# Kernel optimization log

Measured on AMD Instinct MI355X. Metric: run time of the kernel, lower is better.

## Reference

```python
import jax, jax.numpy as jnp
import numpy as np

B, P, S, D, H, DFF, VOC = 16, 10, 128, 512, 8, 2048, 32000
SIGMA = 0.05
LN_EPS = 1e-6


def _ln(x, g, b):
    mu = jnp.mean(x, axis=-1, keepdims=True)
    var = jnp.var(x, axis=-1, keepdims=True)
    return g * (x - mu) / jnp.sqrt(var + LN_EPS) + b


def setup_inputs() -> dict:
    key = jax.random.key(0)
    ks = jax.random.split(key, 16)
    def wmat(k, shp):
        return (jax.random.normal(k, shp) * 0.02).astype(jnp.float32)
    return {
        "r": jax.random.normal(ks[0], (B, P, D), jnp.float32),
        "x": jax.random.randint(ks[1], (B,), 0, VOC),
        "K": jax.random.normal(ks[2], (B, P, S, D), jnp.float32),
        "V": jax.random.normal(ks[3], (B, P, S, D), jnp.float32),
        "w_state": jax.random.uniform(ks[4], (B, P, 1), jnp.float32),
        "I": jax.random.randint(ks[5], (B, P, S), 0, P),
        "t": 64,
        "Wq": wmat(ks[6], (D, D)), "bq": jnp.zeros((D,), jnp.float32),
        "Wk": wmat(ks[7], (D, D)), "bk": jnp.zeros((D,), jnp.float32),
        "Wv": wmat(ks[8], (D, D)), "bv": jnp.zeros((D,), jnp.float32),
        "Wo": wmat(ks[9], (D, D)), "bo": jnp.zeros((D,), jnp.float32),
        "W1": wmat(ks[10], (D, DFF)), "b1": jnp.zeros((DFF,), jnp.float32),
        "W2": wmat(ks[11], (DFF, D)), "b2": jnp.zeros((D,), jnp.float32),
        "g1": jnp.ones((D,), jnp.float32), "be1": jnp.zeros((D,), jnp.float32),
        "g3": jnp.ones((D,), jnp.float32), "be3": jnp.zeros((D,), jnp.float32),
        "Wout": wmat(ks[12], (D, VOC)), "bout": jnp.zeros((VOC,), jnp.float32),
    }


def reference(r, x, K, V, w_state, I, t, Wq, bq, Wk, bk, Wv, bv, Wo, bo,
              W1, b1, W2, b2, g1, be1, g3, be3, Wout, bout):
    k1, k2, k3, k4, k5 = jax.random.split(jax.random.key(42), 5)
    I = I.astype(jnp.int32)
    # particle resampling of attention state: gather along particle dim per timestep
    K = jnp.take_along_axis(K, I[..., None], axis=1)  # (B,P,S,D)
    V = jnp.take_along_axis(V, I[..., None], axis=1)
    rin = r[:, :, None, :]                            # (B,P,1,D)
    q = rin @ Wq + bq
    k = rin @ Wk + bk
    v = rin @ Wv + bv
    # SMC reparameterization noise on the projections
    q = q + SIGMA * jax.random.normal(k1, q.shape, q.dtype)
    k = k + SIGMA * jax.random.normal(k2, k.shape, k.dtype)
    v = v + SIGMA * jax.random.normal(k3, v.shape, v.dtype)
    # write current k, v into the attention state at position t
    K = jax.lax.dynamic_update_slice_in_dim(K, k, t, axis=2)
    V = jax.lax.dynamic_update_slice_in_dim(V, v, t, axis=2)
    dh = D // H
    qh = q.reshape(B, P, 1, H, dh).transpose(0, 1, 3, 2, 4)  # (B,P,H,1,dh)
    Kh = K.reshape(B, P, S, H, dh).transpose(0, 1, 3, 2, 4)  # (B,P,H,S,dh)
    Vh = V.reshape(B, P, S, H, dh).transpose(0, 1, 3, 2, 4)
    scores = jnp.einsum('bphqd,bphsd->bphqs', qh, Kh) / jnp.sqrt(jnp.asarray(dh, q.dtype))
    attn = jax.nn.softmax(scores, axis=-1)                   # (B,P,H,1,S)
    ctx = jnp.einsum('bphqs,bphsd->bphqd', attn, Vh)
    ctx = ctx.transpose(0, 1, 3, 2, 4).reshape(B, P, 1, D)
    z = ctx @ Wo + bo
    epsilon = SIGMA * jax.random.normal(k4, z.shape, z.dtype)  # stored stddev
    z = z + epsilon
    attn_weights = jnp.mean(attn, axis=2)                    # (B,P,1,S)
    out1 = _ln(z + rin, g1, be1)
    ffn = jax.nn.relu(out1 @ W1 + b1) @ W2 + b2
    out3 = _ln(ffn + out1, g3, be3)                          # (B,P,1,D)
    predictions = out3 @ Wout + bout                         # (B,P,1,VOC)
    # classification weight computation: softmax + gather at label x
    probs = jax.nn.softmax(predictions, axis=-1)
    w = jnp.take_along_axis(probs, x[:, None, None, None].astype(jnp.int32), axis=-1)[..., 0, 0]  # (B,P)
    w = jax.lax.stop_gradient(w)
    pred_sq = predictions[:, :, 0, :]                        # (B,P,VOC)
    average_prediction = jnp.sum(pred_sq * w[:, :, None], axis=1)[:, None, :]  # (B,1,VOC)
    argmax_w = jnp.argmax(w, axis=1)
    max_prediction = jnp.take_along_axis(pred_sq, argmax_w[:, None, None], axis=1)[:, 0, :]  # (B,VOC)
    # sample-and-keep-indices: categorical draw of P particle ancestors per batch
    i_t = jax.random.categorical(k5, w[:, None, :], axis=-1, shape=(B, P)).astype(jnp.int32)
    I_new = jax.lax.dynamic_update_slice_in_dim(I, i_t[:, :, None], t, axis=2)
    I_new = jax.lax.stop_gradient(I_new)
    # resample z with the freshly-sampled indices (I_new[:,:,t] == i_t)
    z = jnp.take_along_axis(z, i_t[:, :, None, None], axis=1)
    return out3, z, average_prediction, max_prediction, epsilon, attn_weights, K, V, w, I_new
```

## Files before the change

kernel.cpp:

```cpp
#include <hip/hip_runtime.h>
#include <cstdint>
#include <cstddef>

#define B_    16
#define P_    10
#define S_    128
#define D_    512
#define H_    8
#define DH_   64
#define DFF_  2048
#define VOC_  32000
#define NROW  160
#define SIGMA 0.05f
#define LN_EPS 1e-6f

struct U2 { uint32_t x, y; };

__host__ __device__ __forceinline__ U2 tf2x32(uint32_t k0, uint32_t k1,
                                              uint32_t x0, uint32_t x1) {
  uint32_t ks[3] = {k0, k1, k0 ^ k1 ^ 0x1BD11BDAu};
  x0 += ks[0]; x1 += ks[1];
  const int R0[4] = {13, 15, 26, 6};
  const int R1[4] = {17, 29, 16, 24};
#pragma unroll
  for (int i = 0; i < 5; ++i) {
    const int* r = (i & 1) ? R1 : R0;
#pragma unroll
    for (int j = 0; j < 4; ++j) {
      x0 += x1;
      x1 = (x1 << r[j]) | (x1 >> (32 - r[j]));
      x1 ^= x0;
    }
    x0 += ks[(i + 1) % 3];
    x1 += ks[(i + 2) % 3] + (uint32_t)(i + 1);
  }
  return {x0, x1};
}

__device__ __forceinline__ uint32_t jax_bits32(uint32_t k0, uint32_t k1, uint32_t j) {
  U2 o = tf2x32(k0, k1, 0u, j);
  return o.x ^ o.y;
}

__device__ __forceinline__ float erfinv32(float x) {
  float w = -log1pf(-x * x);
  float p;
  if (w < 5.0f) {
    w = w - 2.5f;
    p = 2.81022636e-08f;
    p = fmaf(p, w, 3.43273939e-07f);
    p = fmaf(p, w, -3.5233877e-06f);
    p = fmaf(p, w, -4.39150654e-06f);
    p = fmaf(p, w, 0.00021858087f);
    p = fmaf(p, w, -0.00125372503f);
    p = fmaf(p, w, -0.00417768164f);
    p = fmaf(p, w, 0.246640727f);
    p = fmaf(p, w, 1.50140941f);
  } else {
    w = sqrtf(w) - 3.0f;
    p = -0.000200214257f;
    p = fmaf(p, w, 0.000100950558f);
    p = fmaf(p, w, 0.00134934322f);
    p = fmaf(p, w, -0.00367342844f);
    p = fmaf(p, w, 0.00573950773f);
    p = fmaf(p, w, -0.0076224613f);
    p = fmaf(p, w, 0.00943887047f);
    p = fmaf(p, w, 1.00167406f);
    p = fmaf(p, w, 2.83297682f);
  }
  return p * x;
}

__device__ __forceinline__ float jax_normal(uint32_t k0, uint32_t k1, uint32_t j) {
  uint32_t b = jax_bits32(k0, k1, j);
  float u01 = __uint_as_float((b >> 9) | 0x3F800000u) - 1.0f;
  const float lo = -0.99999994f;
  float u = fmaxf(lo, fmaf(u01, 2.0f, lo));
  return 1.41421356f * erfinv32(u);
}

__device__ __forceinline__ float jax_gumbel(uint32_t k0, uint32_t k1, uint32_t j) {
  uint32_t b = jax_bits32(k0, k1, j);
  float u01 = __uint_as_float((b >> 9) | 0x3F800000u) - 1.0f;
  const float tiny = 1.17549435e-38f;
  float u = fmaxf(tiny, u01 + tiny);
  return -logf(-logf(u));
}


__global__ __launch_bounds__(256) void k_gather(const float* __restrict__ K,
                                                const float* __restrict__ V,
                                                const int* __restrict__ I,
                                                float* __restrict__ oK,
                                                float* __restrict__ oV) {
  size_t idx = (size_t)blockIdx.x * 256 + threadIdx.x;
  const size_t total = (size_t)NROW * S_ * (D_ / 4);
  if (idx >= total) return;
  int d4 = (int)(idx % (D_ / 4));
  size_t row = idx / (D_ / 4);
  int s = (int)(row % S_);
  int bp = (int)(row / S_);
  int b = bp / P_;
  int iv = I[row];
  size_t src = ((size_t)(b * P_ + iv) * S_ + s) * (D_ / 4) + d4;
  ((float4*)oK)[idx] = ((const float4*)K)[src];
  ((float4*)oV)[idx] = ((const float4*)V)[src];
}

__global__ __launch_bounds__(128) void k_qkvp(const float* __restrict__ r,
    const float* __restrict__ Wq, const float* __restrict__ bq,
    const float* __restrict__ Wk, const float* __restrict__ bk,
    const float* __restrict__ Wv, const float* __restrict__ bv,
    float* __restrict__ pq, float* __restrict__ pk, float* __restrict__ pv) {
  int c = blockIdx.x * 128 + threadIdx.x;
  int r0 = blockIdx.y * 4;
  int kc = blockIdx.z;
  int d0 = kc * 64;
  float aq[4], ak[4], av[4];
  float bbq = (kc == 0) ? bq[c] : 0.f;
  float bbk = (kc == 0) ? bk[c] : 0.f;
  float bbv = (kc == 0) ? bv[c] : 0.f;
#pragma unroll
  for (int rr = 0; rr < 4; ++rr) { aq[rr] = bbq; ak[rr] = bbk; av[rr] = bbv; }
  for (int d = d0; d < d0 + 64; d += 4) {
    float wq0 = Wq[(size_t)d * D_ + c],      wq1 = Wq[(size_t)(d+1) * D_ + c];
    float wq2 = Wq[(size_t)(d+2) * D_ + c],  wq3 = Wq[(size_t)(d+3) * D_ + c];
    float wk0 = Wk[(size_t)d * D_ + c],      wk1 = Wk[(size_t)(d+1) * D_ + c];
    float wk2 = Wk[(size_t)(d+2) * D_ + c],  wk3 = Wk[(size_t)(d+3) * D_ + c];
    float wv0 = Wv[(size_t)d * D_ + c],      wv1 = Wv[(size_t)(d+1) * D_ + c];
    float wv2 = Wv[(size_t)(d+2) * D_ + c],  wv3 = Wv[(size_t)(d+3) * D_ + c];
#pragma unroll
    for (int rr = 0; rr < 4; ++rr) {
      float4 a = *(const float4*)&r[(size_t)(r0 + rr) * D_ + d];
      aq[rr] = fmaf(a.w, wq3, fmaf(a.z, wq2, fmaf(a.y, wq1, fmaf(a.x, wq0, aq[rr]))));
      ak[rr] = fmaf(a.w, wk3, fmaf(a.z, wk2, fmaf(a.y, wk1, fmaf(a.x, wk0, ak[rr]))));
      av[rr] = fmaf(a.w, wv3, fmaf(a.z, wv2, fmaf(a.y, wv1, fmaf(a.x, wv0, av[rr]))));
    }
  }
#pragma unroll
  for (int rr = 0; rr < 4; ++rr) {
    size_t o = ((size_t)kc * NROW + r0 + rr) * D_ + c;
    pq[o] = aq[rr]; pk[o] = ak[rr]; pv[o] = av[rr];
  }
}

__global__ __launch_bounds__(256) void k_qkvr(const float* __restrict__ pq,
    const float* __restrict__ pk, const float* __restrict__ pv,
    const int* __restrict__ tptr, float* __restrict__ wsq,
    float* __restrict__ oK, float* __restrict__ oV,
    uint32_t k1a, uint32_t k1b, uint32_t k2a, uint32_t k2b,
    uint32_t k3a, uint32_t k3b) {
  int idx = blockIdx.x * 256 + threadIdx.x;
  if (idx >= NROW * D_) return;
  float q = pq[idx], k = pk[idx], v = pv[idx];
#pragma unroll
  for (int kc = 1; kc < 8; ++kc) {
    size_t o = (size_t)kc * (NROW * D_) + idx;
    q += pq[o]; k += pk[o]; v += pv[o];
  }
  int bp = idx / D_, c = idx % D_;
  int ts = min(max(*tptr, 0), S_ - 1);
  uint32_t j = (uint32_t)idx;
  wsq[idx] = q + SIGMA * jax_normal(k1a, k1b, j);
  oK[((size_t)bp * S_ + ts) * D_ + c] = k + SIGMA * jax_normal(k2a, k2b, j);
  oV[((size_t)bp * S_ + ts) * D_ + c] = v + SIGMA * jax_normal(k3a, k3b, j);
}

__global__ __launch_bounds__(128) void k_attn(const float* __restrict__ wsq,
    const float* __restrict__ oK, const float* __restrict__ oV,
    float* __restrict__ wsctx, float* __restrict__ wsattn) {
  __shared__ float s_q[DH_];
  __shared__ float s_attn[S_];
  __shared__ float red[S_];
  int bp = blockIdx.x >> 3, h = blockIdx.x & 7, tid = threadIdx.x;
  if (tid < DH_) s_q[tid] = wsq[bp * D_ + h * DH_ + tid];
  __syncthreads();
  const float4* krow = (const float4*)(oK + ((size_t)bp * S_ + tid) * D_ + h * DH_);
  const float4* q4 = (const float4*)s_q;
  float sc = 0.f;
#pragma unroll
  for (int d = 0; d < DH_ / 4; ++d) {
    float4 kv = krow[d], qv = q4[d];
    sc += qv.x * kv.x + qv.y * kv.y + qv.z * kv.z + qv.w * kv.w;
  }
  sc *= 0.125f;
  red[tid] = sc; __syncthreads();
  for (int s = 64; s > 0; s >>= 1) {
    if (tid < s) red[tid] = fmaxf(red[tid], red[tid + s]);
    __syncthreads();
  }
  float m = red[0]; __syncthreads();
  float e = expf(sc - m);
  red[tid] = e; __syncthreads();
  for (int s = 64; s > 0; s >>= 1) {
    if (tid < s) red[tid] += red[tid + s];
    __syncthreads();
  }
  float a = e / red[0];
  s_attn[tid] = a;
  wsattn[(size_t)blockIdx.x * S_ + tid] = a;
  __syncthreads();
  {
    int dd = tid & 63, sh = tid >> 6;
    const float* vb = oV + ((size_t)bp * S_ + sh * 64) * D_ + h * DH_ + dd;
    float acc = 0.f;
#pragma unroll 4
    for (int s = 0; s < 64; ++s) acc = fmaf(s_attn[sh * 64 + s], vb[(size_t)s * D_], acc);
    red[tid] = acc; __syncthreads();
    if (tid < DH_) wsctx[bp * D_ + h * DH_ + tid] = red[tid] + red[tid + 64];
  }
}

__global__ __launch_bounds__(256) void k_aw(const float* __restrict__ wsattn,
                                            float* __restrict__ oaw) {
  int idx = blockIdx.x * 256 + threadIdx.x;
  if (idx >= NROW * S_) return;
  int bp = idx / S_, s = idx % S_;
  float acc = 0.f;
#pragma unroll
  for (int h = 0; h < H_; ++h) acc += wsattn[(size_t)(bp * H_ + h) * S_ + s];
  oaw[idx] = acc * 0.125f;
}

__global__ __launch_bounds__(128) void k_zmatp(const float* __restrict__ wsctx,
    const float* __restrict__ Wo, const float* __restrict__ bo,
    float* __restrict__ pz) {
  int c = blockIdx.x * 128 + threadIdx.x;
  int r0 = blockIdx.y * 4;
  int kc = blockIdx.z;
  int d0 = kc * 64;
  float acc[4];
  float bb = (kc == 0) ? bo[c] : 0.f;
#pragma unroll
  for (int rr = 0; rr < 4; ++rr) acc[rr] = bb;
  for (int d = d0; d < d0 + 64; d += 4) {
    float w0 = Wo[(size_t)d * D_ + c],     w1 = Wo[(size_t)(d+1) * D_ + c];
    float w2 = Wo[(size_t)(d+2) * D_ + c], w3 = Wo[(size_t)(d+3) * D_ + c];
#pragma unroll
    for (int rr = 0; rr < 4; ++rr) {
      float4 a = *(const float4*)&wsctx[(size_t)(r0 + rr) * D_ + d];
      acc[rr] = fmaf(a.w, w3, fmaf(a.z, w2, fmaf(a.y, w1, fmaf(a.x, w0, acc[rr]))));
    }
  }
#pragma unroll
  for (int rr = 0; rr < 4; ++rr)
    pz[((size_t)kc * NROW + r0 + rr) * D_ + c] = acc[rr];
}

__global__ __launch_bounds__(256) void k_zmatr(const float* __restrict__ pz,
    const float* __restrict__ r, float* __restrict__ oeps,
    float* __restrict__ wsz, float* __restrict__ wsx,
    uint32_t k4a, uint32_t k4b) {
  int idx = blockIdx.x * 256 + threadIdx.x;
  if (idx >= NROW * D_) return;
  float s = pz[idx];
#pragma unroll
  for (int kc = 1; kc < 8; ++kc) s += pz[(size_t)kc * (NROW * D_) + idx];
  uint32_t j = (uint32_t)idx;
  float eps = SIGMA * jax_normal(k4a, k4b, j);
  oeps[idx] = eps;
  float z = s + eps;
  wsz[idx] = z;
  wsx[idx] = z + r[idx];
}

__global__ __launch_bounds__(256) void k_ln(const float* __restrict__ wsx,
    const float* __restrict__ g, const float* __restrict__ b,
    float* __restrict__ o) {
  __shared__ float red[256];
  int bp = blockIdx.x, tid = threadIdx.x;
  float x0 = wsx[bp * D_ + tid], x1 = wsx[bp * D_ + tid + 256];
  red[tid] = x0 + x1; __syncthreads();
  for (int s = 128; s > 0; s >>= 1) { if (tid < s) red[tid] += red[tid + s]; __syncthreads(); }
  float mu = red[0] / (float)D_; __syncthreads();
  float d0 = x0 - mu, d1 = x1 - mu;
  red[tid] = d0 * d0 + d1 * d1; __syncthreads();
  for (int s = 128; s > 0; s >>= 1) { if (tid < s) red[tid] += red[tid + s]; __syncthreads(); }
  float inv = 1.0f / sqrtf(red[0] / (float)D_ + LN_EPS);
  o[bp * D_ + tid] = g[tid] * d0 * inv + b[tid];
  o[bp * D_ + tid + 256] = g[tid + 256] * d1 * inv + b[tid + 256];
}

__global__ __launch_bounds__(128) void k_ffn1p(const float* __restrict__ wsout1,
    const float* __restrict__ W1, const float* __restrict__ b1,
    float* __restrict__ pf) {
  int c = blockIdx.x * 128 + threadIdx.x;
  int r0 = blockIdx.y * 8;
  int kc = blockIdx.z;
  int d0 = kc * 128;
  float acc[8];
  float bb = (kc == 0) ? b1[c] : 0.f;
#pragma unroll
  for (int rr = 0; rr < 8; ++rr) acc[rr] = bb;
  for (int d = d0; d < d0 + 128; d += 4) {
    float w0 = W1[(size_t)d * DFF_ + c],     w1 = W1[(size_t)(d+1) * DFF_ + c];
    float w2 = W1[(size_t)(d+2) * DFF_ + c], w3 = W1[(size_t)(d+3) * DFF_ + c];
#pragma unroll
    for (int rr = 0; rr < 8; ++rr) {
      float4 a = *(const float4*)&wsout1[(size_t)(r0 + rr) * D_ + d];
      acc[rr] = fmaf(a.w, w3, fmaf(a.z, w2, fmaf(a.y, w1, fmaf(a.x, w0, acc[rr]))));
    }
  }
#pragma unroll
  for (int rr = 0; rr < 8; ++rr)
    pf[((size_t)kc * NROW + r0 + rr) * DFF_ + c] = acc[rr];
}

__global__ __launch_bounds__(256) void k_ffn1r(const float* __restrict__ pf,
    float* __restrict__ wsffn) {
  int idx = blockIdx.x * 256 + threadIdx.x;
  if (idx >= NROW * DFF_) return;
  float s = pf[idx];
#pragma unroll
  for (int kc = 1; kc < 4; ++kc) s += pf[(size_t)kc * (NROW * DFF_) + idx];
  wsffn[idx] = fmaxf(s, 0.f);
}

__global__ __launch_bounds__(128) void k_ffn2p(const float* __restrict__ wsffn,
    const float* __restrict__ W2, float* __restrict__ p2) {
  int c = blockIdx.x * 128 + threadIdx.x;
  int r0 = blockIdx.y * 4;
  int kc = blockIdx.z;
  int d0 = kc * 128;
  float acc[4];
#pragma unroll
  for (int rr = 0; rr < 4; ++rr) acc[rr] = 0.f;
  for (int d = d0; d < d0 + 128; d += 4) {
    float w0 = W2[(size_t)d * D_ + c],     w1 = W2[(size_t)(d+1) * D_ + c];
    float w2 = W2[(size_t)(d+2) * D_ + c], w3 = W2[(size_t)(d+3) * D_ + c];
#pragma unroll
    for (int rr = 0; rr < 4; ++rr) {
      float4 a = *(const float4*)&wsffn[(size_t)(r0 + rr) * DFF_ + d];
      acc[rr] = fmaf(a.w, w3, fmaf(a.z, w2, fmaf(a.y, w1, fmaf(a.x, w0, acc[rr]))));
    }
  }
#pragma unroll
  for (int rr = 0; rr < 4; ++rr)
    p2[((size_t)kc * NROW + r0 + rr) * D_ + c] = acc[rr];
}

__global__ __launch_bounds__(256) void k_ffn2r(const float* __restrict__ p2,
    const float* __restrict__ b2, const float* __restrict__ wsout1,
    float* __restrict__ wsx) {
  int idx = blockIdx.x * 256 + threadIdx.x;
  if (idx >= NROW * D_) return;
  float s = p2[idx];
#pragma unroll
  for (int kc = 1; kc < 16; ++kc) s += p2[(size_t)kc * (NROW * D_) + idx];
  int c = idx % D_;
  wsx[idx] = s + b2[c] + wsout1[idx];
}

__global__ __launch_bounds__(256, 3) void k_preds(const float* __restrict__ A,
    const float* __restrict__ Wout, const float* __restrict__ bout,
    float* __restrict__ wspred) {
  __shared__ float sA[NROW][68];
  int tid = threadIdx.x;
  int cb = blockIdx.x;
  int cg = tid & 7, rg = tid >> 3;
  int c = cb * 64 + cg * 8;
  float4 acc[5][2];
  {
    float4 b0 = *(const float4*)&bout[c];
    float4 b1 = *(const float4*)&bout[c + 4];
#pragma unroll
    for (int i = 0; i < 5; ++i) { acc[i][0] = b0; acc[i][1] = b1; }
  }
  for (int d0 = 0; d0 < D_; d0 += 64) {
    if (d0) __syncthreads();
#pragma unroll
    for (int k = 0; k < 10; ++k) {
      int idx = tid + k * 256;
      int row = idx >> 4, c4 = idx & 15;
      *(float4*)&sA[row][c4 * 4] =
          *(const float4*)&A[(size_t)row * D_ + d0 + c4 * 4];
    }
    __syncthreads();
#pragma unroll 2
    for (int dd = 0; dd < 64; dd += 4) {
      size_t wb = (size_t)(d0 + dd) * VOC_ + c;
      float4 w00 = *(const float4*)&Wout[wb];
      float4 w01 = *(const float4*)&Wout[wb + 4];
      float4 w10 = *(const float4*)&Wout[wb + VOC_];
      float4 w11 = *(const float4*)&Wout[wb + VOC_ + 4];
      float4 w20 = *(const float4*)&Wout[wb + 2 * (size_t)VOC_];
      float4 w21 = *(const float4*)&Wout[wb + 2 * (size_t)VOC_ + 4];
      float4 w30 = *(const float4*)&Wout[wb + 3 * (size_t)VOC_];
      float4 w31 = *(const float4*)&Wout[wb + 3 * (size_t)VOC_ + 4];
#define FMA8(av, wA, wB)                                   \
      acc[i][0].x = fmaf(av, wA.x, acc[i][0].x);           \
      acc[i][0].y = fmaf(av, wA.y, acc[i][0].y);           \
      acc[i][0].z = fmaf(av, wA.z, acc[i][0].z);           \
      acc[i][0].w = fmaf(av, wA.w, acc[i][0].w);           \
      acc[i][1].x = fmaf(av, wB.x, acc[i][1].x);           \
      acc[i][1].y = fmaf(av, wB.y, acc[i][1].y);           \
      acc[i][1].z = fmaf(av, wB.z, acc[i][1].z);           \
      acc[i][1].w = fmaf(av, wB.w, acc[i][1].w);
#pragma unroll
      for (int i = 0; i < 5; ++i) {
        float4 a = *(const float4*)&sA[rg * 5 + i][dd];
        FMA8(a.x, w00, w01)
        FMA8(a.y, w10, w11)
        FMA8(a.z, w20, w21)
        FMA8(a.w, w30, w31)
      }
#undef FMA8
    }
  }
#pragma unroll
  for (int i = 0; i < 5; ++i) {
    size_t o = (size_t)(rg * 5 + i) * VOC_ + c;
    *(float4*)&wspred[o] = acc[i][0];
    *(float4*)&wspred[o + 4] = acc[i][1];
  }
}

__global__ __launch_bounds__(256) void k_stats(const float* __restrict__ wspred,
    const int* __restrict__ x, float* __restrict__ ow) {
  __shared__ float red[256];
  int bp = blockIdx.x, tid = threadIdx.x;
  const float* row = wspred + (size_t)bp * VOC_;
  const float4* row4 = (const float4*)row;
  float m = -INFINITY;
  for (int i = tid; i < VOC_ / 4; i += 256) {
    float4 v = row4[i];
    m = fmaxf(m, fmaxf(fmaxf(v.x, v.y), fmaxf(v.z, v.w)));
  }
  red[tid] = m; __syncthreads();
  for (int s = 128; s > 0; s >>= 1) { if (tid < s) red[tid] = fmaxf(red[tid], red[tid + s]); __syncthreads(); }
  m = red[0]; __syncthreads();
  float sum = 0.f;
  for (int i = tid; i < VOC_ / 4; i += 256) {
    float4 v = row4[i];
    sum += expf(v.x - m) + expf(v.y - m) + expf(v.z - m) + expf(v.w - m);
  }
  red[tid] = sum; __syncthreads();
  for (int s = 128; s > 0; s >>= 1) { if (tid < s) red[tid] += red[tid + s]; __syncthreads(); }
  if (tid == 0) {
    int b = bp / P_;
    ow[bp] = expf(row[x[b]] - m) / red[0];
  }
}

__global__ __launch_bounds__(256) void k_it(const float* __restrict__ ow,
    int* __restrict__ wsit, int* __restrict__ wsamw,
    uint32_t k5a, uint32_t k5b) {
  int tid = threadIdx.x;
  if (tid < NROW) {
    int b = tid / P_;
    float best = -INFINITY; int bi = 0;
#pragma unroll
    for (int i = 0; i < P_; ++i) {
      float g = jax_gumbel(k5a, k5b, (uint32_t)(tid * P_ + i));
      float v = g + ow[b * P_ + i];
      if (v > best) { best = v; bi = i; }
    }
    wsit[tid] = bi;
  }
  if (tid < B_) {
    float best = -INFINITY; int bi = 0;
#pragma unroll
    for (int p = 0; p < P_; ++p) {
      float v = ow[tid * P_ + p];
      if (v > best) { best = v; bi = p; }
    }
    wsamw[tid] = bi;
  }
}

__global__ __launch_bounds__(256) void k_avgmax(const float* __restrict__ wspred,
    const float* __restrict__ ow, const int* __restrict__ wsamw,
    float* __restrict__ oavg, float* __restrict__ omax) {
  int idx = blockIdx.x * 256 + threadIdx.x;
  if (idx >= B_ * VOC_) return;
  int b = idx / VOC_, c = idx % VOC_;
  float acc = 0.f;
#pragma unroll
  for (int p = 0; p < P_; ++p)
    acc = fmaf(wspred[(size_t)(b * P_ + p) * VOC_ + c], ow[b * P_ + p], acc);
  oavg[idx] = acc;
  omax[idx] = wspred[(size_t)(b * P_ + wsamw[b]) * VOC_ + c];
}

__global__ __launch_bounds__(256) void k_zsel(const float* __restrict__ wsz,
    const int* __restrict__ wsit, const int* __restrict__ I,
    const int* __restrict__ tptr, float* __restrict__ oz, float* __restrict__ oI) {
  int idx = blockIdx.x * 256 + threadIdx.x;
  if (idx < NROW * D_) {
    int bp = idx / D_, d = idx % D_;
    int b = bp / P_;
    oz[idx] = wsz[(size_t)(b * P_ + wsit[bp]) * D_ + d];
  }
  if (idx < NROW * S_) {
    int bp = idx / S_, s = idx % S_;
    int ts = min(max(*tptr, 0), S_ - 1);
    oI[idx] = (s == ts) ? (float)wsit[bp] : (float)I[idx];
  }
}

static void derive_keys(uint32_t keys[5][2]) {
  for (int i = 0; i < 5; ++i) {
    U2 o = tf2x32(0u, 42u, 0u, (uint32_t)i);
    keys[i][0] = o.x; keys[i][1] = o.y;
  }
}

extern "C" void kernel_launch(void* const* d_in, const int* in_sizes, int n_in,
                              void* d_out, int out_size, void* d_ws, size_t ws_size,
                              hipStream_t stream) {
  const float* r   = (const float*)d_in[0];
  const int*   x   = (const int*)d_in[1];
  const float* K   = (const float*)d_in[2];
  const float* V   = (const float*)d_in[3];
  const int*   I   = (const int*)d_in[5];
  const int*   tp  = (const int*)d_in[6];
  const float* Wq  = (const float*)d_in[7];
  const float* bq  = (const float*)d_in[8];
  const float* Wk  = (const float*)d_in[9];
  const float* bk  = (const float*)d_in[10];
  const float* Wv  = (const float*)d_in[11];
  const float* bv  = (const float*)d_in[12];
  const float* Wo  = (const float*)d_in[13];
  const float* bo  = (const float*)d_in[14];
  const float* W1  = (const float*)d_in[15];
  const float* b1  = (const float*)d_in[16];
  const float* W2  = (const float*)d_in[17];
  const float* b2  = (const float*)d_in[18];
  const float* g1  = (const float*)d_in[19];
  const float* be1 = (const float*)d_in[20];
  const float* g3  = (const float*)d_in[21];
  const float* be3 = (const float*)d_in[22];
  const float* Wout = (const float*)d_in[23];
  const float* bout = (const float*)d_in[24];

  float* out = (float*)d_out;
  const size_t O_OUT3 = 0;
  const size_t O_Z    = 81920;
  const size_t O_AVG  = 163840;
  const size_t O_MAX  = 675840;
  const size_t O_EPS  = 1187840;
  const size_t O_AW   = 1269760;
  const size_t O_K    = 1290240;
  const size_t O_V    = 11776000;
  const size_t O_W    = 22261760;
  const size_t O_I    = 22261920;

  float* ws = (float*)d_ws;
  const size_t W_Q    = 0;
  const size_t W_CTX  = 81920;
  const size_t W_Z    = 163840;
  const size_t W_OUT1 = 245760;
  const size_t W_ATT  = 327680;
  const size_t W_FFN  = 491520;
  const size_t W_PRED = 819200;
  const size_t W_IT   = 5939200;
  const size_t W_AMW  = 5939360;
  const size_t W_X    = W_Q;

  uint32_t kk[5][2];
  derive_keys(kk);

  float* oK = out + O_K;
  float* oV = out + O_V;
  float* sc = ws + W_PRED;

  k_gather<<<10240, 256, 0, stream>>>(K, V, I, oK, oV);
  k_qkvp<<<dim3(4, 40, 8), 128, 0, stream>>>(r, Wq, bq, Wk, bk, Wv, bv,
                                             sc, sc + 655360, sc + 1310720);
  k_qkvr<<<320, 256, 0, stream>>>(sc, sc + 655360, sc + 1310720, tp,
                                  ws + W_Q, oK, oV,
                                  kk[0][0], kk[0][1], kk[1][0], kk[1][1],
                                  kk[2][0], kk[2][1]);
  k_attn<<<NROW * H_, 128, 0, stream>>>(ws + W_Q, oK, oV, ws + W_CTX, ws + W_ATT);
  k_aw<<<(NROW * S_ + 255) / 256, 256, 0, stream>>>(ws + W_ATT, out + O_AW);
  k_zmatp<<<dim3(4, 40, 8), 128, 0, stream>>>(ws + W_CTX, Wo, bo, sc);
  k_zmatr<<<320, 256, 0, stream>>>(sc, r, out + O_EPS, ws + W_Z, ws + W_X,
                                   kk[3][0], kk[3][1]);
  k_ln<<<NROW, 256, 0, stream>>>(ws + W_X, g1, be1, ws + W_OUT1);
  k_ffn1p<<<dim3(16, 20, 4), 128, 0, stream>>>(ws + W_OUT1, W1, b1, sc);
  k_ffn1r<<<1280, 256, 0, stream>>>(sc, ws + W_FFN);
  k_ffn2p<<<dim3(4, 40, 16), 128, 0, stream>>>(ws + W_FFN, W2, sc);
  k_ffn2r<<<320, 256, 0, stream>>>(sc, b2, ws + W_OUT1, ws + W_X);
  k_ln<<<NROW, 256, 0, stream>>>(ws + W_X, g3, be3, out + O_OUT3);
  k_preds<<<dim3(500), 256, 0, stream>>>(out + O_OUT3, Wout, bout, ws + W_PRED);
  k_stats<<<NROW, 256, 0, stream>>>(ws + W_PRED, x, out + O_W);
  k_it<<<1, 256, 0, stream>>>(out + O_W, (int*)(ws + W_IT), (int*)(ws + W_AMW),
                              kk[4][0], kk[4][1]);
  k_avgmax<<<(B_ * VOC_ + 255) / 256, 256, 0, stream>>>(ws + W_PRED, out + O_W,
                                                        (const int*)(ws + W_AMW),
                                                        out + O_AVG, out + O_MAX);
  k_zsel<<<(NROW * D_ + 255) / 256, 256, 0, stream>>>(ws + W_Z, (const int*)(ws + W_IT),
                                                      I, tp, out + O_Z, out + O_I);
}
```

Baseline: 450.1 us.

## Split vocab projection rows across grid and K across two in-block teams

The output-projection GEMM now launches a 2D grid, with each block handling 80 of the 160 rows. Inside a block, two 128-thread teams each cover half of the 512-deep reduction and combine partial sums through shared memory. Shared-memory tiles shrink so occupancy can rise to four blocks per CU. The aim is more parallelism and latency hiding on the Wout stream, but Wout is now read twice (once per row half), and there are extra barriers and a shared-memory reduction step.

Result: no change. 453.0 us (+0.6%).

```diff
diff --git a/kernel.cpp b/kernel.cpp
--- a/kernel.cpp
+++ b/kernel.cpp
@@ -351,42 +351,53 @@
   wsx[idx] = s + b2[c] + wsout1[idx];
 }
 
-__global__ __launch_bounds__(256, 3) void k_preds(const float* __restrict__ A,
+__global__ __launch_bounds__(256, 4) void k_preds(const float* __restrict__ A,
     const float* __restrict__ Wout, const float* __restrict__ bout,
     float* __restrict__ wspred) {
-  __shared__ float sA[NROW][68];
+  __shared__ float sA[2][80][36];
   int tid = threadIdx.x;
-  int cb = blockIdx.x;
-  int cg = tid & 7, rg = tid >> 3;
+  int team = tid >> 7;
+  int lt = tid & 127;
+  int cg = lt & 7;
+  int rg = lt >> 3;
+  int cb = blockIdx.x, rh = blockIdx.y;
   int c = cb * 64 + cg * 8;
+  const float* Ab = A + (size_t)rh * 80 * D_;
+  const float* Wp = Wout + c;
   float4 acc[5][2];
-  {
+  if (team == 0) {
     float4 b0 = *(const float4*)&bout[c];
     float4 b1 = *(const float4*)&bout[c + 4];
 #pragma unroll
     for (int i = 0; i < 5; ++i) { acc[i][0] = b0; acc[i][1] = b1; }
-  }
-  for (int d0 = 0; d0 < D_; d0 += 64) {
-    if (d0) __syncthreads();
-#pragma unroll
-    for (int k = 0; k < 10; ++k) {
-      int idx = tid + k * 256;
-      int row = idx >> 4, c4 = idx & 15;
-      *(float4*)&sA[row][c4 * 4] =
-          *(const float4*)&A[(size_t)row * D_ + d0 + c4 * 4];
+  } else {
+    float4 z = {0.f, 0.f, 0.f, 0.f};
+#pragma unroll
+    for (int i = 0; i < 5; ++i) { acc[i][0] = z; acc[i][1] = z; }
+  }
+  const int dbase = team * 256;
+  for (int ch = 0; ch < 8; ++ch) {
+    int d0 = dbase + ch * 32;
+    if (ch) __syncthreads();
+#pragma unroll
+    for (int k = 0; k < 5; ++k) {
+      int idx = lt + k * 128;
+      int row = idx >> 3, c4 = idx & 7;
+      *(float4*)&sA[team][row][c4 * 4] =
+          *(const float4*)&Ab[(size_t)row * D_ + d0 + c4 * 4];
     }
     __syncthreads();
 #pragma unroll 2
-    for (int dd = 0; dd < 64; dd += 4) {
-      size_t wb = (size_t)(d0 + dd) * VOC_ + c;
-      float4 w00 = *(const float4*)&Wout[wb];
-      float4 w01 = *(const float4*)&Wout[wb + 4];
-      float4 w10 = *(const float4*)&Wout[wb + VOC_];
-      float4 w11 = *(const float4*)&Wout[wb + VOC_ + 4];
-      float4 w20 = *(const float4*)&Wout[wb + 2 * (size_t)VOC_];
-      float4 w21 = *(const float4*)&Wout[wb + 2 * (size_t)VOC_ + 4];
-      float4 w30 = *(const float4*)&Wout[wb + 3 * (size_t)VOC_];
-      float4 w31 = *(const float4*)&Wout[wb + 3 * (size_t)VOC_ + 4];
+    for (int dd = 0; dd < 32; dd += 4) {
+      size_t wb = (size_t)(d0 + dd) * VOC_;
+      float4 w00 = *(const float4*)&Wp[wb];
+      float4 w01 = *(const float4*)&Wp[wb + 4];
+      float4 w10 = *(const float4*)&Wp[wb + VOC_];
+      float4 w11 = *(const float4*)&Wp[wb + VOC_ + 4];
+      float4 w20 = *(const float4*)&Wp[wb + 2 * (size_t)VOC_];
+      float4 w21 = *(const float4*)&Wp[wb + 2 * (size_t)VOC_ + 4];
+      float4 w30 = *(const float4*)&Wp[wb + 3 * (size_t)VOC_];
+      float4 w31 = *(const float4*)&Wp[wb + 3 * (size_t)VOC_ + 4];
 #define FMA8(av, wA, wB)                                   \
       acc[i][0].x = fmaf(av, wA.x, acc[i][0].x);           \
       acc[i][0].y = fmaf(av, wA.y, acc[i][0].y);           \
@@ -398,7 +409,7 @@
       acc[i][1].w = fmaf(av, wB.w, acc[i][1].w);
 #pragma unroll
       for (int i = 0; i < 5; ++i) {
-        float4 a = *(const float4*)&sA[rg * 5 + i][dd];
+        float4 a = *(const float4*)&sA[team][rg * 5 + i][dd];
         FMA8(a.x, w00, w01)
         FMA8(a.y, w10, w11)
         FMA8(a.z, w20, w21)
@@ -407,11 +418,29 @@
 #undef FMA8
     }
   }
-#pragma unroll
-  for (int i = 0; i < 5; ++i) {
-    size_t o = (size_t)(rg * 5 + i) * VOC_ + c;
-    *(float4*)&wspred[o] = acc[i][0];
-    *(float4*)&wspred[o + 4] = acc[i][1];
+  __syncthreads();
+  float* ex = &sA[0][0][0];
+  if (team == 1) {
+#pragma unroll
+    for (int i = 0; i < 5; ++i) {
+      *(float4*)&ex[lt * 40 + i * 8]     = acc[i][0];
+      *(float4*)&ex[lt * 40 + i * 8 + 4] = acc[i][1];
+    }
+  }
+  __syncthreads();
+  if (team == 0) {
+#pragma unroll
+    for (int i = 0; i < 5; ++i) {
+      float4 h0 = *(const float4*)&ex[lt * 40 + i * 8];
+      float4 h1 = *(const float4*)&ex[lt * 40 + i * 8 + 4];
+      acc[i][0].x += h0.x; acc[i][0].y += h0.y;
+      acc[i][0].z += h0.z; acc[i][0].w += h0.w;
+      acc[i][1].x += h1.x; acc[i][1].y += h1.y;
+      acc[i][1].z += h1.z; acc[i][1].w += h1.w;
+      size_t o = (size_t)(rh * 80 + rg * 5 + i) * VOC_ + c;
+      *(float4*)&wspred[o] = acc[i][0];
+      *(float4*)&wspred[o + 4] = acc[i][1];
+    }
   }
 }
 
@@ -582,7 +611,7 @@
   k_ffn2p<<<dim3(4, 40, 16), 128, 0, stream>>>(ws + W_FFN, W2, sc);
   k_ffn2r<<<320, 256, 0, stream>>>(sc, b2, ws + W_OUT1, ws + W_X);
   k_ln<<<NROW, 256, 0, stream>>>(ws + W_X, g3, be3, out + O_OUT3);
-  k_preds<<<dim3(500), 256, 0, stream>>>(out + O_OUT3, Wout, bout, ws + W_PRED);
+  k_preds<<<dim3(500, 2), 256, 0, stream>>>(out + O_OUT3, Wout, bout, ws + W_PRED);
   k_stats<<<NROW, 256, 0, stream>>>(ws + W_PRED, x, out + O_W);
   k_it<<<1, 256, 0, stream>>>(out + O_W, (int*)(ws + W_IT), (int*)(ws + W_AMW),
                               kk[4][0], kk[4][1]);
```
